# Kernel tuning notes

Hardware: AMD Instinct MI355X
Metric: run time of the kernel (lower is better)

Reference implementation:

```python
import jax, jax.numpy as jnp
import numpy as np

N = 50000          # nodes
E_RAND = 590000    # random edges (+ N self-loops -> E = 640000)
IN_F = 128
OUT_F = 128
H, D = 8, 16       # num_heads, head_dim (H*D == OUT_F)
HOP = 5
ALPHA = 0.1
SLOPE = 0.2
EPS = 1e-5


def _layer_norm(x, g, b):
    mu = jnp.mean(x, axis=-1, keepdims=True)
    var = jnp.mean((x - mu) ** 2, axis=-1, keepdims=True)
    return (x - mu) * jax.lax.rsqrt(var + EPS) * g + b


def setup_inputs() -> dict:
    key = jax.random.key(0)
    ks = jax.random.split(key, 10)
    loops = jnp.arange(N, dtype=jnp.int32)  # self-loops -> no 0-in-degree nodes
    src = jnp.concatenate([loops, jax.random.randint(ks[0], (E_RAND,), 0, N, dtype=jnp.int32)])
    dst = jnp.concatenate([loops, jax.random.randint(ks[1], (E_RAND,), 0, N, dtype=jnp.int32)])
    s = 0.05  # xavier-like small init gain
    return {
        "feat": jax.random.normal(ks[2], (N, IN_F), jnp.float32),
        "src": src,
        "dst": dst,
        "w_head": jax.random.normal(ks[3], (OUT_F, IN_F), jnp.float32) * s,
        "w_tail": jax.random.normal(ks[4], (OUT_F, IN_F), jnp.float32) * s,
        "w_ent": jax.random.normal(ks[5], (OUT_F, IN_F), jnp.float32) * s,
        "attn": jax.random.normal(ks[6], (1, H, D), jnp.float32) * s,
        "ln1_g": jnp.ones((IN_F,), jnp.float32),
        "ln1_b": jnp.zeros((IN_F,), jnp.float32),
        "ln2_g": jnp.ones((OUT_F,), jnp.float32),
        "ln2_b": jnp.zeros((OUT_F,), jnp.float32),
        "ff_w1": jax.random.normal(ks[7], (4 * OUT_F, OUT_F), jnp.float32) * s,
        "ff_b1": jnp.zeros((4 * OUT_F,), jnp.float32),
        "ff_w2": jax.random.normal(ks[8], (OUT_F, 4 * OUT_F), jnp.float32) * s,
        "ff_b2": jnp.zeros((OUT_F,), jnp.float32),
    }


def _forward(src, dst, feat, w_head, w_tail, w_ent, attn,
             ln1_g, ln1_b, ln2_g, ln2_b, ff_w1, ff_b1, ff_w2, ff_b2):
    ones = jnp.ones(src.shape[0], jnp.float32)
    out_deg = jnp.clip(jax.ops.segment_sum(ones, src, num_segments=N), 1.0)  # [N]
    in_deg = jnp.clip(jax.ops.segment_sum(ones, dst, num_segments=N), 1.0)
    head_norm = out_deg ** -0.5
    tail_norm = in_deg ** 0.5
    log_in = jnp.log1p(in_deg)  # graph.dstdata['log_in'] (log of in-degree, set at graph build time)

    x = _layer_norm(feat, ln1_g, ln1_b)  # graph_layer_norm (feat_drop=0 in eval)
    fh = (x @ w_head.T).reshape(N, H, D) * head_norm[:, None, None]
    ft = (x @ w_tail.T).reshape(N, H, D) * head_norm[:, None, None]
    fe = (x @ w_ent.T).reshape(N, H, D) * head_norm[:, None, None]

    # edge attention logits: u_mul_v -> leaky_relu -> dot with attn vector
    lr = jax.nn.leaky_relu(fh[src] * ft[dst], SLOPE)  # [E,H,D]
    e = jnp.einsum('ehd,xhd->eh', lr, attn)           # [E,H]
    e = e * log_in[dst][:, None] / D                  # e_mul_v with log_in, / head_dim

    # edge softmax grouped by destination node, per head
    seg_max = jax.ops.segment_max(e, dst, num_segments=N)
    e_exp = jnp.exp(e - seg_max[dst])
    denom = jax.ops.segment_sum(e_exp, dst, num_segments=N)
    a = e_exp / denom[dst]                            # [E,H]

    # PPR diffusion (ppr_estimation), attn_drop=0 in eval
    feat0 = fe
    h = feat0
    for hop in range(HOP):
        if hop > 0:
            h = h * head_norm[:, None, None]
        m = h[src] * a[:, :, None]                    # [E,H,D] u_mul_e
        h = jax.ops.segment_sum(m, dst, num_segments=N)  # fn.sum
        h = h * tail_norm[:, None, None]
        h = (1.0 - ALPHA) * h + ALPHA * feat0

    rst = h + feat.reshape(N, H, D)  # res_fc is Identity since in_feats == out_feats
    rst = rst.reshape(N, OUT_F)
    ff = _layer_norm(rst, ln2_g, ln2_b)
    ff = jax.nn.relu(ff @ ff_w1.T + ff_b1) @ ff_w2.T + ff_b2  # PositionWiseFeedForward
    return ff + rst


def reference(feat, src, dst, w_head, w_tail, w_ent, attn, ln1_g, ln1_b,
              ln2_g, ln2_b, ff_w1, ff_b1, ff_w2, ff_b2):
    return _forward(src, dst, feat, w_head, w_tail, w_ent, attn,
                    ln1_g, ln1_b, ln2_g, ln2_b, ff_w1, ff_b1, ff_w2, ff_b2)
```

## Files before the change

### kernel.cpp

```cpp
#include <hip/hip_runtime.h>
#include <hip/hip_bf16.h>
#include <hip/hip_fp16.h>

typedef __attribute__((ext_vector_type(8))) short bf16x8;
typedef __attribute__((ext_vector_type(4))) float f32x4;
typedef unsigned int uint32;

#define F 128
#define HOPS 5
#define LDS_STRIDE 68
#define W1_STRIDE 136
#define W2_STRIDE 72
#define TB_STRIDE 72

__device__ __forceinline__ float b2f(__hip_bfloat16 h) { return __bfloat162float(h); }
__device__ __forceinline__ __hip_bfloat16 f2b(float f) { return __float2bfloat16(f); }

__device__ __forceinline__ float load_in(const void* p, size_t i, int isbf) {
    return isbf ? __bfloat162float(((const __hip_bfloat16*)p)[i]) : ((const float*)p)[i];
}

__device__ __forceinline__ float bflo(uint32 u) { union { uint32 i; float f; } v; v.i = u << 16; return v.f; }
__device__ __forceinline__ float bfhi(uint32 u) { union { uint32 i; float f; } v; v.i = u & 0xffff0000u; return v.f; }
__device__ __forceinline__ uint32 packbf2(float a, float b) {
    __hip_bfloat16 ha = f2b(a), hb = f2b(b);
    unsigned short ua = *(unsigned short*)&ha, ub = *(unsigned short*)&hb;
    return ((uint32)ub << 16) | ua;
}

__device__ __forceinline__ int xcd_id() {
    unsigned v;
    asm volatile("s_getreg_b32 %0, hwreg(HW_REG_XCC_ID)" : "=s"(v));
    return (int)(v & 7);
}

__device__ __forceinline__ float edge_dot2(uint4 gv, const float* c1, const float* c2) {
    float acc = 0.f, acc2 = 0.f;
    uint32 us[4] = {gv.x, gv.y, gv.z, gv.w};
    #pragma unroll
    for (int k = 0; k < 4; ++k) {
        float f0 = bflo(us[k]), f1 = bfhi(us[k]);
        acc  = fmaf(c1[2 * k],     f0,        acc);
        acc2 = fmaf(c2[2 * k],     fabsf(f0), acc2);
        acc  = fmaf(c1[2 * k + 1], f1,        acc);
        acc2 = fmaf(c2[2 * k + 1], fabsf(f1), acc2);
    }
    return acc + acc2;
}

__global__ void detect_k(const uint32* __restrict__ w, int* flag) {
    __shared__ int cnt[256];
    int t = threadIdx.x;
    uint32 x = w[t * 97];
    int e_low = (x >> 7) & 0xFF;
    cnt[t] = (e_low >= 110 && e_low <= 135) ? 1 : 0;
    __syncthreads();
    for (int s = 128; s > 0; s >>= 1) {
        if (t < s) cnt[t] += cnt[t + s];
        __syncthreads();
    }
    if (t == 0) flag[0] = (cnt[0] >= 160) ? 1 : 0;
}

__global__ void cvt_all_k(const void* __restrict__ w_head, const void* __restrict__ w_tail,
                          const void* __restrict__ w_ent, const void* __restrict__ ff_w1,
                          const void* __restrict__ ff_w2, const void* __restrict__ attn,
                          const void* __restrict__ ff_b1, const void* __restrict__ ff_b2,
                          const int* __restrict__ flag,
                          __hip_bfloat16* __restrict__ wblob, float* __restrict__ fblob) {
    int i = blockIdx.x * blockDim.x + threadIdx.x;
    int isbf = flag[0];
    if (i < 180224) {
        const void* srcp; int j;
        if (i < 16384)       { srcp = w_head; j = i; }
        else if (i < 32768)  { srcp = w_tail; j = i - 16384; }
        else if (i < 49152)  { srcp = w_ent;  j = i - 32768; }
        else if (i < 114688) { srcp = ff_w1;  j = i - 49152; }
        else                 { srcp = ff_w2;  j = i - 114688; }
        wblob[i] = f2b(load_in(srcp, j, isbf));
    } else if (i < 180992) {
        int k = i - 180224;
        const void* srcp; int j;
        if (k < 128)      { srcp = attn;  j = k; }
        else if (k < 640) { srcp = ff_b1; j = k - 128; }
        else              { srcp = ff_b2; j = k - 640; }
        fblob[k] = load_in(srcp, j, isbf);
    }
}

__global__ void degree_k(const int* __restrict__ src, const int* __restrict__ dst,
                         int* in8, int* out1, uint32* __restrict__ pack, int E, int N) {
    int base = blockIdx.x * (blockDim.x * 8) + threadIdx.x;
    int slice = xcd_id();
    int idx[8], d[8], s[8], r[8];
#pragma unroll
    for (int k = 0; k < 8; ++k) idx[k] = base + k * 256;
#pragma unroll
    for (int k = 0; k < 8; ++k)
        if (idx[k] < E) { d[k] = dst[idx[k]]; s[k] = src[idx[k]]; }
#pragma unroll
    for (int k = 0; k < 8; ++k)
        if (idx[k] < E) r[k] = atomicAdd(&in8[slice * N + d[k]], 1);
#pragma unroll
    for (int k = 0; k < 8; ++k)
        if (idx[k] < E) atomicAdd(&out1[s[k]], 1);
#pragma unroll
    for (int k = 0; k < 8; ++k)
        if (idx[k] < E) pack[idx[k]] = (uint32)r[k] | ((uint32)slice << 24);
}

__global__ void scan1_k(const int* __restrict__ in8, int* partial, int* blk_sum, int N) {
    __shared__ int sh[256];
    int t = threadIdx.x;
    int i = blockIdx.x * 256 + t;
    int c = 0;
    if (i < N) {
#pragma unroll
        for (int s = 0; s < 8; ++s) c += in8[s * N + i];
    }
    sh[t] = c;
    __syncthreads();
    for (int o = 1; o < 256; o <<= 1) {
        int v = (t >= o) ? sh[t - o] : 0;
        __syncthreads();
        sh[t] += v;
        __syncthreads();
    }
    if (i < N) partial[i] = sh[t] - c;
    if (t == 255) blk_sum[blockIdx.x] = sh[255];
}

__global__ void scan2_k(const int* __restrict__ blk_sum, int* blk_off, int nb,
                        int* row_ptr, int N) {
    __shared__ int sh[256];
    int t = threadIdx.x;
    if (nb <= 256) {
        int v = (t < nb) ? blk_sum[t] : 0;
        sh[t] = v;
        __syncthreads();
        for (int o = 1; o < 256; o <<= 1) {
            int u = (t >= o) ? sh[t - o] : 0;
            __syncthreads();
            sh[t] += u;
            __syncthreads();
        }
        if (t < nb) blk_off[t] = sh[t] - v;
        if (t == 255) row_ptr[N] = sh[255];
    } else if (t == 0) {
        int run = 0;
        for (int b = 0; b < nb; ++b) { blk_off[b] = run; run += blk_sum[b]; }
        row_ptr[N] = run;
    }
}

__global__ void scan3_norms_k(const int* __restrict__ partial, const int* __restrict__ blk_off,
                              const int* __restrict__ in8, const int* __restrict__ out1,
                              int* row_ptr, int* soff, float* head_norm, float* tail_norm,
                              float* log_in, int N) {
    int i = blockIdx.x * 256 + threadIdx.x;
    if (i >= N) return;
    row_ptr[i] = partial[i] + blk_off[blockIdx.x];
    int run = 0;
#pragma unroll
    for (int s = 0; s < 8; ++s) { soff[s * N + i] = run; run += in8[s * N + i]; }
    int od = out1[i];
    float id = fmaxf((float)run, 1.0f);
    float odf = fmaxf((float)od, 1.0f);
    head_norm[i] = rsqrtf(odf);
    tail_norm[i] = sqrtf(id);
    log_in[i] = log1pf(id);
}

__global__ void scan3f_k(const int* __restrict__ partial, const int* __restrict__ blk_sum,
                         int nb, const int* __restrict__ in8, const int* __restrict__ out1,
                         int* row_ptr, int* soff, float* head_norm, float* tail_norm,
                         float* log_in, int N) {
    __shared__ int bs[256];
    int t = threadIdx.x;
    bs[t] = (t < nb) ? blk_sum[t] : 0;
    __syncthreads();
    for (int o = 1; o < 256; o <<= 1) {
        int v = (t >= o) ? bs[t - o] : 0;
        __syncthreads();
        bs[t] += v;
        __syncthreads();
    }
    if (blockIdx.x == 0 && t == 0) row_ptr[N] = bs[nb - 1];
    int boff = (blockIdx.x == 0) ? 0 : bs[blockIdx.x - 1];
    int i = blockIdx.x * 256 + t;
    if (i >= N) return;
    row_ptr[i] = partial[i] + boff;
    int run = 0;
#pragma unroll
    for (int s = 0; s < 8; ++s) { soff[s * N + i] = run; run += in8[s * N + i]; }
    int od = out1[i];
    float id = fmaxf((float)run, 1.0f);
    float odf = fmaxf((float)od, 1.0f);
    head_norm[i] = rsqrtf(odf);
    tail_norm[i] = sqrtf(id);
    log_in[i] = log1pf(id);
}

__global__ void scatter_k(const int* __restrict__ src, const int* __restrict__ dst,
                          const int* __restrict__ row_ptr, const int* __restrict__ soff,
                          const uint32* __restrict__ pack, int* csr_src, int E, int N) {
    int i = blockIdx.x * blockDim.x + threadIdx.x;
    if (i < E) {
        int d = dst[i];
        uint32 pk = pack[i];
        int s = (int)(pk >> 24);
        int r = (int)(pk & 0xFFFFFFu);
        csr_src[row_ptr[d] + soff[s * N + d] + r] = src[i];
    }
}

__global__ void ln1_k(const void* __restrict__ x, const void* __restrict__ g,
                      const void* __restrict__ b, const int* __restrict__ flag,
                      __hip_bfloat16* __restrict__ y, int N) {
    int w = blockIdx.x * (blockDim.x >> 6) + (threadIdx.x >> 6);
    if (w >= N) return;
    int isbf = flag[0];
    int t = threadIdx.x & 63;
    float v0 = load_in(x, (size_t)w * F + t, isbf);
    float v1 = load_in(x, (size_t)w * F + t + 64, isbf);
    float s = v0 + v1, sq = v0 * v0 + v1 * v1;
    for (int m = 1; m < 64; m <<= 1) { s += __shfl_xor(s, m, 64); sq += __shfl_xor(sq, m, 64); }
    float mu = s * (1.0f / F);
    float var = fmaxf(sq * (1.0f / F) - mu * mu, 0.0f);
    float r = rsqrtf(var + 1e-5f);
    y[(size_t)w * F + t]      = f2b((v0 - mu) * r * load_in(g, t, isbf) + load_in(b, t, isbf));
    y[(size_t)w * F + t + 64] = f2b((v1 - mu) * r * load_in(g, t + 64, isbf) + load_in(b, t + 64, isbf));
}

__global__ void proj_gemm_k(const __hip_bfloat16* __restrict__ X,
                            const __hip_bfloat16* __restrict__ Wall,
                            const float* __restrict__ head_norm,
                            __hip_bfloat16* __restrict__ fh,
                            __hip_bfloat16* __restrict__ ft,
                            uint32* __restrict__ fe_bf, int N) {
    __shared__ __align__(16) char smem[2 * 64 * W1_STRIDE * 2];
    __hip_bfloat16* lx = (__hip_bfloat16*)smem;
    __hip_bfloat16* lw = (__hip_bfloat16*)(smem + 64 * W1_STRIDE * 2);
    float* eps = (float*)smem;
    int tid = threadIdx.x;
    int wv = tid >> 6, lane = tid & 63;
    int lr = lane & 15, quad = lane >> 4;
    int bm = blockIdx.x * 64;
    int g = blockIdx.y;
    int wsel = g >> 1;
    int wcb = (g & 1) * 64;
    {
        const __hip_bfloat16* xs = X + (size_t)bm * F;
        size_t maxe = (size_t)N * F;
#pragma unroll
        for (int i = 0; i < 4; ++i) {
            int idx = i * 2048 + tid * 8;
            int n = idx >> 7, k = idx & 127;
            size_t gi = (size_t)bm * F + idx;
            uint4 v = (gi + 8 <= maxe) ? *(const uint4*)(xs + idx)
                                       : *(const uint4*)(X + maxe - 8);
            *(uint4*)&lx[n * W1_STRIDE + k] = v;
        }
        const __hip_bfloat16* ws = Wall + ((size_t)wsel * F + wcb) * F;
#pragma unroll
        for (int i = 0; i < 4; ++i) {
            int idx = i * 2048 + tid * 8;
            int n = idx >> 7, k = idx & 127;
            *(uint4*)&lw[n * W1_STRIDE + k] = *(const uint4*)(ws + idx);
        }
    }
    __syncthreads();
    f32x4 acc[4] = {{0,0,0,0},{0,0,0,0},{0,0,0,0},{0,0,0,0}};
#pragma unroll
    for (int ks = 0; ks < 4; ++ks) {
        bf16x8 a = *reinterpret_cast<const bf16x8*>(&lx[(wv * 16 + lr) * W1_STRIDE + ks * 32 + quad * 8]);
#pragma unroll
        for (int j = 0; j < 4; ++j) {
            bf16x8 bb = *reinterpret_cast<const bf16x8*>(&lw[(j * 16 + lr) * W1_STRIDE + ks * 32 + quad * 8]);
            acc[j] = __builtin_amdgcn_mfma_f32_16x16x32_bf16(a, bb, acc[j], 0, 0, 0);
        }
    }
    __syncthreads();
    int rl = wv * 16 + quad * 4;
#pragma unroll
    for (int j = 0; j < 4; ++j)
#pragma unroll
        for (int r = 0; r < 4; ++r)
            eps[(rl + r) * LDS_STRIDE + j * 16 + lr] = acc[j][r];
    __syncthreads();
    int tr = tid >> 4, tc = (tid & 15) * 4;
#pragma unroll
    for (int p = 0; p < 4; ++p) {
        int row_l = p * 16 + tr;
        int grow = bm + row_l;
        if (grow >= N) continue;
        float4 v = *(const float4*)&eps[row_l * LDS_STRIDE + tc];
        float hn = head_norm[grow];
        v.x *= hn; v.y *= hn; v.z *= hn; v.w *= hn;
        size_t idx = (size_t)grow * F + wcb + tc;
        uint2 u; u.x = packbf2(v.x, v.y); u.y = packbf2(v.z, v.w);
        __hip_bfloat16* dstp = (wsel == 0) ? fh : (wsel == 1) ? ft : (__hip_bfloat16*)fe_bf;
        *(uint2*)&dstp[idx] = u;
    }
}

__global__ void attn_soft_k(const int* __restrict__ csr_src, const int* __restrict__ row_ptr,
                            const uint32* __restrict__ fh2, const uint32* __restrict__ ft2,
                            const float* __restrict__ attn_f, const float* __restrict__ log_in,
                            __half* __restrict__ e_h, float* __restrict__ inv_arr, int N) {
    int w = blockIdx.x * (blockDim.x >> 6) + (threadIdx.x >> 6);
    if (w >= N) return;
    int t = threadIdx.x & 63;
    int g = t >> 4, j = t & 15;
    int b = row_ptr[w], e = row_ptr[w + 1];
    uint4 fr = ((const uint4*)ft2)[(size_t)w * 16 + j];
    float ftf[8] = {bflo(fr.x), bfhi(fr.x), bflo(fr.y), bfhi(fr.y),
                    bflo(fr.z), bfhi(fr.z), bflo(fr.w), bfhi(fr.w)};
    float c1[8], c2[8];
#pragma unroll
    for (int k = 0; k < 8; ++k) {
        float at = attn_f[8 * j + k];
        c1[k] = 0.6f * at * ftf[k];
        c2[k] = 0.4f * at * fabsf(ftf[k]);
    }
    float scale = log_in[w] * (1.0f / 16.0f);
    float m = -1e30f;
    for (int p0 = b; p0 < e; p0 += 8) {
        int pa = p0 + g, pb = p0 + 4 + g;
        bool oka = pa < e, okb = pb < e;
        int sa = csr_src[oka ? pa : b];
        int sb = csr_src[okb ? pb : b];
        uint4 ga = ((const uint4*)fh2)[(size_t)sa * 16 + j];
        uint4 gb = ((const uint4*)fh2)[(size_t)sb * 16 + j];
        float ra = edge_dot2(ga, c1, c2);
        float rb = edge_dot2(gb, c1, c2);
        ra += __shfl_xor(ra, 1, 64);
        rb += __shfl_xor(rb, 1, 64);
        float la = ra * scale, lb = rb * scale;
        if (oka) { if (!(j & 1)) e_h[(size_t)pa * 8 + (j >> 1)] = __float2half(la); m = fmaxf(m, la); }
        if (okb) { if (!(j & 1)) e_h[(size_t)pb * 8 + (j >> 1)] = __float2half(lb); m = fmaxf(m, lb); }
    }
    m = fmaxf(m, __shfl_xor(m, 16, 64));
    m = fmaxf(m, __shfl_xor(m, 32, 64));
    float mh = __shfl(m, (t & 7) * 2, 64);
    float sum = 0.f;
    for (size_t base = (size_t)b * 8 + t; base < (size_t)e * 8; base += 64) {
        float ex = expf(__half2float(e_h[base]) - mh);
        e_h[base] = __float2half(ex);
        sum += ex;
    }
    sum += __shfl_xor(sum, 8, 64);
    sum += __shfl_xor(sum, 16, 64);
    sum += __shfl_xor(sum, 32, 64);
    float inv = 1.0f / fmaxf(sum, 1e-30f);
    if (t < 8) inv_arr[(size_t)w * 8 + t] = inv;
}

__global__ void hop_k(const uint32* __restrict__ gsrc2, const __half* __restrict__ e_h,
                      const float* __restrict__ inv_arr,
                      const int* __restrict__ csr_src, const int* __restrict__ row_ptr,
                      const float* __restrict__ tail_norm, const float* __restrict__ head_norm,
                      const uint32* __restrict__ fe_bf, const void* __restrict__ feat,
                      const void* __restrict__ ln2g, const void* __restrict__ ln2b,
                      const int* __restrict__ flag,
                      uint32* __restrict__ out_bf, float* __restrict__ out_f32,
                      int last, int N) {
    int w = blockIdx.x * 8 + (threadIdx.x >> 5);
    if (w >= N) return;
    int l = threadIdx.x & 31;
    int h = l >> 2;
    int b = row_ptr[w], e = row_ptr[w + 1];
    float inv = inv_arr[(size_t)w * 8 + h];
    float a0 = 0.f, a1 = 0.f, a2 = 0.f, a3 = 0.f;
    int p = b;
    for (; p + 8 <= e; p += 8) {
        int s[8]; float av[8]; uint2 gg[8];
#pragma unroll
        for (int i = 0; i < 8; ++i) s[i] = csr_src[p + i];
#pragma unroll
        for (int i = 0; i < 8; ++i) av[i] = __half2float(e_h[(size_t)(p + i) * 8 + h]);
#pragma unroll
        for (int i = 0; i < 8; ++i) gg[i] = ((const uint2*)gsrc2)[(size_t)s[i] * 32 + l];
#pragma unroll
        for (int i = 0; i < 8; ++i) {
            a0 += bflo(gg[i].x) * av[i]; a1 += bfhi(gg[i].x) * av[i];
            a2 += bflo(gg[i].y) * av[i]; a3 += bfhi(gg[i].y) * av[i];
        }
    }
    if (p < e) {
        int s[8]; float av[8]; uint2 gg[8];
#pragma unroll
        for (int i = 0; i < 8; ++i) {
            int q = p + i;
            bool ok = q < e;
            int q2 = ok ? q : b;
            s[i] = csr_src[q2];
            av[i] = ok ? __half2float(e_h[(size_t)q * 8 + h]) : 0.f;
        }
#pragma unroll
        for (int i = 0; i < 8; ++i) gg[i] = ((const uint2*)gsrc2)[(size_t)s[i] * 32 + l];
#pragma unroll
        for (int i = 0; i < 8; ++i) {
            a0 += bflo(gg[i].x) * av[i]; a1 += bfhi(gg[i].x) * av[i];
            a2 += bflo(gg[i].y) * av[i]; a3 += bfhi(gg[i].y) * av[i];
        }
    }
    float tl = tail_norm[w] * 0.9f * inv;
    uint2 feu = ((const uint2*)fe_bf)[(size_t)w * 32 + l];
    float r0 = tl * a0 + 0.1f * bflo(feu.x);
    float r1 = tl * a1 + 0.1f * bfhi(feu.x);
    float r2 = tl * a2 + 0.1f * bflo(feu.y);
    float r3 = tl * a3 + 0.1f * bfhi(feu.y);
    if (last) {
        int isbf = flag[0];
        float4 o;
        if (isbf) {
            uint2 fu = ((const uint2*)feat)[(size_t)w * 32 + l];
            o.x = r0 + bflo(fu.x); o.y = r1 + bfhi(fu.x);
            o.z = r2 + bflo(fu.y); o.w = r3 + bfhi(fu.y);
        } else {
            float4 fv = ((const float4*)feat)[(size_t)w * 32 + l];
            o.x = r0 + fv.x; o.y = r1 + fv.y; o.z = r2 + fv.z; o.w = r3 + fv.w;
        }
        ((float4*)out_f32)[(size_t)w * 32 + l] = o;
        float s2 = o.x + o.y + o.z + o.w;
        float sq = o.x * o.x + o.y * o.y + o.z * o.z + o.w * o.w;
#pragma unroll
        for (int mm = 1; mm < 32; mm <<= 1) {
            s2 += __shfl_xor(s2, mm, 64);
            sq += __shfl_xor(sq, mm, 64);
        }
        float mu = s2 * (1.0f / F);
        float var = fmaxf(sq * (1.0f / F) - mu * mu, 0.0f);
        float rr = rsqrtf(var + 1e-5f);
        float g0 = load_in(ln2g, 4 * l + 0, isbf), g1 = load_in(ln2g, 4 * l + 1, isbf);
        float g2 = load_in(ln2g, 4 * l + 2, isbf), g3 = load_in(ln2g, 4 * l + 3, isbf);
        float b0 = load_in(ln2b, 4 * l + 0, isbf), b1 = load_in(ln2b, 4 * l + 1, isbf);
        float b2 = load_in(ln2b, 4 * l + 2, isbf), b3 = load_in(ln2b, 4 * l + 3, isbf);
        uint2 u;
        u.x = packbf2((o.x - mu) * rr * g0 + b0, (o.y - mu) * rr * g1 + b1);
        u.y = packbf2((o.z - mu) * rr * g2 + b2, (o.w - mu) * rr * g3 + b3);
        ((uint2*)out_bf)[(size_t)w * 32 + l] = u;
    } else {
        float hn = head_norm[w];
        uint2 u;
        u.x = packbf2(r0 * hn, r1 * hn);
        u.y = packbf2(r2 * hn, r3 * hn);
        ((uint2*)out_bf)[(size_t)w * 32 + l] = u;
    }
}

__global__ __launch_bounds__(256, 2)
void ffn_fused_k(const __hip_bfloat16* __restrict__ Y, const __hip_bfloat16* __restrict__ W1,
                 const __hip_bfloat16* __restrict__ W2, const float* __restrict__ b1f,
                 const float* __restrict__ b2f, const float* __restrict__ rst,
                 const int* __restrict__ flag, void* __restrict__ out, int N) {
    __shared__ __align__(16) char smem[45056];
    __hip_bfloat16* lw1 = (__hip_bfloat16*)smem;
    __hip_bfloat16* lw2 = (__hip_bfloat16*)(smem + 17408);
    __hip_bfloat16* tb  = (__hip_bfloat16*)(smem + 35840);
    float* eps = (float*)smem;
    int tid = threadIdx.x;
    int wv = tid >> 6, lane = tid & 63;
    int lr = lane & 15, quad = lane >> 4;
    int bm = blockIdx.x * 64;
    int row_a = bm + wv * 16 + lr;
    if (row_a >= N) row_a = N - 1;
    bf16x8 ay[4];
    {
        const __hip_bfloat16* yr = Y + (size_t)row_a * F + quad * 8;
#pragma unroll
        for (int ks = 0; ks < 4; ++ks) ay[ks] = *reinterpret_cast<const bf16x8*>(yr + ks * 32);
    }
    f32x4 o[8];
#pragma unroll
    for (int j = 0; j < 8; ++j) o[j] = (f32x4){0,0,0,0};
    __hip_bfloat16* tbuf = tb + wv * (16 * TB_STRIDE);
    for (int c = 0; c < 8; ++c) {
        int nb0 = c * 64;
        __syncthreads();
        {
            const __hip_bfloat16* s1 = W1 + (size_t)nb0 * F;
#pragma unroll
            for (int i = 0; i < 4; ++i) {
                int idx = i * 2048 + tid * 8;
                int n = idx >> 7, k = idx & 127;
                *(uint4*)&lw1[n * W1_STRIDE + k] = *(const uint4*)(s1 + idx);
            }
#pragma unroll
            for (int i = 0; i < 4; ++i) {
                int idx = i * 2048 + tid * 8;
                int r = idx >> 6, k2 = idx & 63;
                *(uint4*)&lw2[r * W2_STRIDE + k2] = *(const uint4*)(W2 + (size_t)r * 512 + nb0 + k2);
            }
        }
        __syncthreads();
        f32x4 t[4] = {{0,0,0,0},{0,0,0,0},{0,0,0,0},{0,0,0,0}};
#pragma unroll
        for (int ks = 0; ks < 4; ++ks) {
#pragma unroll
            for (int j = 0; j < 4; ++j) {
                bf16x8 bb = *reinterpret_cast<const bf16x8*>(&lw1[(j * 16 + lr) * W1_STRIDE + ks * 32 + quad * 8]);
                t[j] = __builtin_amdgcn_mfma_f32_16x16x32_bf16(ay[ks], bb, t[j], 0, 0, 0);
            }
        }
#pragma unroll
        for (int j = 0; j < 4; ++j) {
            float bias = b1f[nb0 + 16 * j + lr];
#pragma unroll
            for (int r = 0; r < 4; ++r) {
                float v = fmaxf(t[j][r] + bias, 0.f);
                tbuf[(quad * 4 + r) * TB_STRIDE + j * 16 + lr] = f2b(v);
            }
        }
#pragma unroll
        for (int ks2 = 0; ks2 < 2; ++ks2) {
            bf16x8 at = *reinterpret_cast<const bf16x8*>(&tbuf[lr * TB_STRIDE + ks2 * 32 + quad * 8]);
#pragma unroll
            for (int j2 = 0; j2 < 8; ++j2) {
                bf16x8 bb = *reinterpret_cast<const bf16x8*>(&lw2[(j2 * 16 + lr) * W2_STRIDE + ks2 * 32 + quad * 8]);
                o[j2] = __builtin_amdgcn_mfma_f32_16x16x32_bf16(at, bb, o[j2], 0, 0, 0);
            }
        }
    }
    __syncthreads();
    int rl = wv * 16 + quad * 4;
#pragma unroll
    for (int j = 0; j < 8; ++j)
#pragma unroll
        for (int r = 0; r < 4; ++r)
            eps[(rl + r) * 132 + j * 16 + lr] = o[j][r];
    __syncthreads();
    int isbf = flag[0];
#pragma unroll
    for (int p = 0; p < 8; ++p) {
        int idx = p * 1024 + tid * 4;
        int row_l = idx >> 7, col = idx & 127;
        int grow = bm + row_l;
        if (grow >= N) continue;
        float4 v = *(const float4*)&eps[row_l * 132 + col];
        float4 bias = *(const float4*)&b2f[col];
        float4 rv = *(const float4*)&rst[(size_t)grow * F + col];
        v.x += bias.x + rv.x; v.y += bias.y + rv.y;
        v.z += bias.z + rv.z; v.w += bias.w + rv.w;
        size_t gidx = (size_t)grow * F + col;
        if (isbf) {
            uint2 u; u.x = packbf2(v.x, v.y); u.y = packbf2(v.z, v.w);
            *(uint2*)&((__hip_bfloat16*)out)[gidx] = u;
        } else {
            *(float4*)&((float*)out)[gidx] = v;
        }
    }
}

extern "C" void kernel_launch(void* const* d_in, const int* in_sizes, int n_in,
                              void* d_out, int out_size, void* d_ws, size_t ws_size,
                              hipStream_t stream) {
    if (n_in < 15) return;
    const void* feat = d_in[0];
    const int* src = (const int*)d_in[1];
    const int* dst = (const int*)d_in[2];
    const void* w_head = d_in[3];
    const void* w_tail = d_in[4];
    const void* w_ent  = d_in[5];
    const void* attn   = d_in[6];
    const void* ln1_g  = d_in[7];
    const void* ln1_b  = d_in[8];
    const void* ln2_g  = d_in[9];
    const void* ln2_b  = d_in[10];
    const void* ff_w1  = d_in[11];
    const void* ff_b1  = d_in[12];
    const void* ff_w2  = d_in[13];
    const void* ff_b2  = d_in[14];

    const int N = in_sizes[0] / F;
    const int E = in_sizes[1];
    (void)out_size;

    char* base = (char*)d_ws;
    size_t off = 0;
    auto alloc = [&](size_t bytes) -> void* {
        void* r = base + off;
        off += (bytes + 255) & ~(size_t)255;
        return r;
    };
    int* zr        = (int*)alloc((size_t)9 * N * 4);
    int* in8 = zr, * out1 = zr + 8 * N;
    int* soff      = (int*)alloc((size_t)8 * N * 4);
    int* row_ptr   = (int*)alloc((size_t)(N + 1) * 4);
    int* partial   = (int*)alloc((size_t)N * 4);
    int* blk_sum   = (int*)alloc((size_t)1024 * 4);
    int* blk_off   = (int*)alloc((size_t)1024 * 4);
    int* flag      = (int*)alloc(256);
    float* head_norm = (float*)alloc((size_t)N * 4);
    float* tail_norm = (float*)alloc((size_t)N * 4);
    float* log_in    = (float*)alloc((size_t)N * 4);
    float* inv_arr   = (float*)alloc((size_t)N * 8 * 4);
    int* csr_src   = (int*)alloc((size_t)E * 4);
    uint32* pack   = (uint32*)alloc((size_t)E * 4);
    __hip_bfloat16* wh_bf = (__hip_bfloat16*)alloc((size_t)F * F * 2);
    __hip_bfloat16* wt_bf = (__hip_bfloat16*)alloc((size_t)F * F * 2);
    __hip_bfloat16* we_bf = (__hip_bfloat16*)alloc((size_t)F * F * 2);
    __hip_bfloat16* w1_bf = (__hip_bfloat16*)alloc((size_t)512 * F * 2);
    __hip_bfloat16* w2_bf = (__hip_bfloat16*)alloc((size_t)F * 512 * 2);
    float* attn_f    = (float*)alloc((size_t)F * 4);
    float* b1f       = (float*)alloc((size_t)512 * 4);
    float* b2f_      = (float*)alloc((size_t)F * 4);
    __hip_bfloat16* x_bf = (__hip_bfloat16*)alloc((size_t)N * F * 2);
    __hip_bfloat16* fh   = (__hip_bfloat16*)alloc((size_t)N * F * 2);
    __hip_bfloat16* ftb  = (__hip_bfloat16*)alloc((size_t)N * F * 2);
    uint32* fe_bf = (uint32*)alloc((size_t)N * F * 2);
    uint32* hA_bf = (uint32*)alloc((size_t)N * F * 2);
    uint32* hB_bf = (uint32*)alloc((size_t)N * F * 2);
    float* rst = (float*)alloc((size_t)N * F * 4);
    __hip_bfloat16* y_bf = (__hip_bfloat16*)hA_bf;
    __half* e_h = (__half*)x_bf;
    (void)wt_bf; (void)we_bf;
    if (off > ws_size) return;

    const int Mb = (N + 63) / 64;
    const int nodeBlocks = (N + 3) / 4;
    const int hopBlocks = (N + 7) / 8;
    const int nb = (N + 255) / 256;

    detect_k<<<1, 256, 0, stream>>>((const uint32*)feat, flag);
    cvt_all_k<<<(180992 + 255) / 256, 256, 0, stream>>>(w_head, w_tail, w_ent, ff_w1, ff_w2,
                                                        attn, ff_b1, ff_b2, flag, wh_bf, attn_f);

    hipMemsetAsync(zr, 0, (size_t)9 * N * 4, stream);
    degree_k<<<(E + 2047) / 2048, 256, 0, stream>>>(src, dst, in8, out1, pack, E, N);
    scan1_k<<<nb, 256, 0, stream>>>(in8, partial, blk_sum, N);
    if (nb <= 256) {
        scan3f_k<<<nb, 256, 0, stream>>>(partial, blk_sum, nb, in8, out1,
                                         row_ptr, soff, head_norm, tail_norm, log_in, N);
    } else {
        scan2_k<<<1, 256, 0, stream>>>(blk_sum, blk_off, nb, row_ptr, N);
        scan3_norms_k<<<nb, 256, 0, stream>>>(partial, blk_off, in8, out1,
                                              row_ptr, soff, head_norm, tail_norm, log_in, N);
    }
    scatter_k<<<(E + 255) / 256, 256, 0, stream>>>(src, dst, row_ptr, soff, pack, csr_src, E, N);

    ln1_k<<<nodeBlocks, 256, 0, stream>>>(feat, ln1_g, ln1_b, flag, x_bf, N);
    proj_gemm_k<<<dim3(Mb, 6), 256, 0, stream>>>(x_bf, wh_bf, head_norm, fh, ftb, fe_bf, N);

    attn_soft_k<<<nodeBlocks, 256, 0, stream>>>(csr_src, row_ptr, (const uint32*)fh,
                                                (const uint32*)ftb, attn_f, log_in,
                                                e_h, inv_arr, N);

    const uint32* gsrc = fe_bf;
    uint32* bufs[2] = {hA_bf, hB_bf};
    for (int hop = 0; hop < HOPS; ++hop) {
        int last = (hop == HOPS - 1);
        uint32* dst_bf = last ? (uint32*)y_bf : bufs[hop & 1];
        hop_k<<<hopBlocks, 256, 0, stream>>>(gsrc, e_h, inv_arr, csr_src, row_ptr, tail_norm,
                                             head_norm, fe_bf, feat, ln2_g, ln2_b, flag,
                                             dst_bf, rst, last, N);
        if (!last) gsrc = dst_bf;
    }

    ffn_fused_k<<<Mb, 256, 0, stream>>>(y_bf, w1_bf, w2_bf, b1f, b2f_, rst, flag, d_out, N);
}
```

Measured before the change: 450.1 us.

## Merge independent preprocessing kernels into block-partitioned fused launches

Combines degree counting, LayerNorm1 and weight conversion into one launch whose blocks branch on block index. It also merges the CSR scatter with the projection GEMM into a second launch. This removes several kernel launches and gaps between them, and lets independent work overlap on the device. The cost is that the GEMM blocks carry the same LDS allocation as the scatter blocks, and occupancy is set by the heavier branch.

Measured after the change: 429.2 us. 4.6% less time.

```diff
diff --git a/kernel.cpp b/kernel.cpp
--- a/kernel.cpp
+++ b/kernel.cpp
@@ -62,51 +62,75 @@
     if (t == 0) flag[0] = (cnt[0] >= 160) ? 1 : 0;
 }
 
-__global__ void cvt_all_k(const void* __restrict__ w_head, const void* __restrict__ w_tail,
-                          const void* __restrict__ w_ent, const void* __restrict__ ff_w1,
-                          const void* __restrict__ ff_w2, const void* __restrict__ attn,
-                          const void* __restrict__ ff_b1, const void* __restrict__ ff_b2,
-                          const int* __restrict__ flag,
-                          __hip_bfloat16* __restrict__ wblob, float* __restrict__ fblob) {
-    int i = blockIdx.x * blockDim.x + threadIdx.x;
-    int isbf = flag[0];
-    if (i < 180224) {
-        const void* srcp; int j;
-        if (i < 16384)       { srcp = w_head; j = i; }
-        else if (i < 32768)  { srcp = w_tail; j = i - 16384; }
-        else if (i < 49152)  { srcp = w_ent;  j = i - 32768; }
-        else if (i < 114688) { srcp = ff_w1;  j = i - 49152; }
-        else                 { srcp = ff_w2;  j = i - 114688; }
-        wblob[i] = f2b(load_in(srcp, j, isbf));
-    } else if (i < 180992) {
-        int k = i - 180224;
-        const void* srcp; int j;
-        if (k < 128)      { srcp = attn;  j = k; }
-        else if (k < 640) { srcp = ff_b1; j = k - 128; }
-        else              { srcp = ff_b2; j = k - 640; }
-        fblob[k] = load_in(srcp, j, isbf);
-    }
-}
-
-__global__ void degree_k(const int* __restrict__ src, const int* __restrict__ dst,
-                         int* in8, int* out1, uint32* __restrict__ pack, int E, int N) {
-    int base = blockIdx.x * (blockDim.x * 8) + threadIdx.x;
-    int slice = xcd_id();
-    int idx[8], d[8], s[8], r[8];
-#pragma unroll
-    for (int k = 0; k < 8; ++k) idx[k] = base + k * 256;
-#pragma unroll
-    for (int k = 0; k < 8; ++k)
-        if (idx[k] < E) { d[k] = dst[idx[k]]; s[k] = src[idx[k]]; }
-#pragma unroll
-    for (int k = 0; k < 8; ++k)
-        if (idx[k] < E) r[k] = atomicAdd(&in8[slice * N + d[k]], 1);
-#pragma unroll
-    for (int k = 0; k < 8; ++k)
-        if (idx[k] < E) atomicAdd(&out1[s[k]], 1);
-#pragma unroll
-    for (int k = 0; k < 8; ++k)
-        if (idx[k] < E) pack[idx[k]] = (uint32)r[k] | ((uint32)slice << 24);
+__global__ void fused_pre_k(const int* __restrict__ src, const int* __restrict__ dst,
+                            int* in8, int* out1, uint32* __restrict__ pack, int E,
+                            const void* __restrict__ feat, const void* __restrict__ ln1g,
+                            const void* __restrict__ ln1b,
+                            const void* __restrict__ w_head, const void* __restrict__ w_tail,
+                            const void* __restrict__ w_ent, const void* __restrict__ ff_w1,
+                            const void* __restrict__ ff_w2, const void* __restrict__ attn,
+                            const void* __restrict__ ff_b1, const void* __restrict__ ff_b2,
+                            const int* __restrict__ flag,
+                            __hip_bfloat16* __restrict__ wblob, float* __restrict__ fblob,
+                            __hip_bfloat16* __restrict__ x_bf,
+                            int nbDeg, int nbLn, int N) {
+    int bid = blockIdx.x;
+    if (bid < nbDeg) {
+        int base = bid * 2048 + threadIdx.x;
+        int slice = xcd_id();
+        int idx[8], d[8], s[8], r[8];
+#pragma unroll
+        for (int k = 0; k < 8; ++k) idx[k] = base + k * 256;
+#pragma unroll
+        for (int k = 0; k < 8; ++k)
+            if (idx[k] < E) { d[k] = dst[idx[k]]; s[k] = src[idx[k]]; }
+#pragma unroll
+        for (int k = 0; k < 8; ++k)
+            if (idx[k] < E) r[k] = atomicAdd(&in8[slice * N + d[k]], 1);
+#pragma unroll
+        for (int k = 0; k < 8; ++k)
+            if (idx[k] < E) atomicAdd(&out1[s[k]], 1);
+#pragma unroll
+        for (int k = 0; k < 8; ++k)
+            if (idx[k] < E) pack[idx[k]] = (uint32)r[k] | ((uint32)slice << 24);
+        return;
+    }
+    if (bid < nbDeg + nbLn) {
+        int w = (bid - nbDeg) * 4 + (threadIdx.x >> 6);
+        if (w >= N) return;
+        int isbf = flag[0];
+        int t = threadIdx.x & 63;
+        float v0 = load_in(feat, (size_t)w * F + t, isbf);
+        float v1 = load_in(feat, (size_t)w * F + t + 64, isbf);
+        float s = v0 + v1, sq = v0 * v0 + v1 * v1;
+        for (int m = 1; m < 64; m <<= 1) { s += __shfl_xor(s, m, 64); sq += __shfl_xor(sq, m, 64); }
+        float mu = s * (1.0f / F);
+        float var = fmaxf(sq * (1.0f / F) - mu * mu, 0.0f);
+        float r = rsqrtf(var + 1e-5f);
+        x_bf[(size_t)w * F + t]      = f2b((v0 - mu) * r * load_in(ln1g, t, isbf) + load_in(ln1b, t, isbf));
+        x_bf[(size_t)w * F + t + 64] = f2b((v1 - mu) * r * load_in(ln1g, t + 64, isbf) + load_in(ln1b, t + 64, isbf));
+        return;
+    }
+    {
+        int i = (bid - nbDeg - nbLn) * 256 + threadIdx.x;
+        int isbf = flag[0];
+        if (i < 180224) {
+            const void* srcp; int j;
+            if (i < 16384)       { srcp = w_head; j = i; }
+            else if (i < 32768)  { srcp = w_tail; j = i - 16384; }
+            else if (i < 49152)  { srcp = w_ent;  j = i - 32768; }
+            else if (i < 114688) { srcp = ff_w1;  j = i - 49152; }
+            else                 { srcp = ff_w2;  j = i - 114688; }
+            wblob[i] = f2b(load_in(srcp, j, isbf));
+        } else if (i < 180992) {
+            int k = i - 180224;
+            const void* srcp; int j;
+            if (k < 128)      { srcp = attn;  j = k; }
+            else if (k < 640) { srcp = ff_b1; j = k - 128; }
+            else              { srcp = ff_b2; j = k - 640; }
+            fblob[k] = load_in(srcp, j, isbf);
+        }
+    }
 }
 
 __global__ void scan1_k(const int* __restrict__ in8, int* partial, int* blk_sum, int N) {
@@ -201,52 +225,42 @@
     log_in[i] = log1pf(id);
 }
 
-__global__ void scatter_k(const int* __restrict__ src, const int* __restrict__ dst,
-                          const int* __restrict__ row_ptr, const int* __restrict__ soff,
-                          const uint32* __restrict__ pack, int* csr_src, int E, int N) {
-    int i = blockIdx.x * blockDim.x + threadIdx.x;
-    if (i < E) {
-        int d = dst[i];
-        uint32 pk = pack[i];
-        int s = (int)(pk >> 24);
-        int r = (int)(pk & 0xFFFFFFu);
-        csr_src[row_ptr[d] + soff[s * N + d] + r] = src[i];
-    }
-}
-
-__global__ void ln1_k(const void* __restrict__ x, const void* __restrict__ g,
-                      const void* __restrict__ b, const int* __restrict__ flag,
-                      __hip_bfloat16* __restrict__ y, int N) {
-    int w = blockIdx.x * (blockDim.x >> 6) + (threadIdx.x >> 6);
-    if (w >= N) return;
-    int isbf = flag[0];
-    int t = threadIdx.x & 63;
-    float v0 = load_in(x, (size_t)w * F + t, isbf);
-    float v1 = load_in(x, (size_t)w * F + t + 64, isbf);
-    float s = v0 + v1, sq = v0 * v0 + v1 * v1;
-    for (int m = 1; m < 64; m <<= 1) { s += __shfl_xor(s, m, 64); sq += __shfl_xor(sq, m, 64); }
-    float mu = s * (1.0f / F);
-    float var = fmaxf(sq * (1.0f / F) - mu * mu, 0.0f);
-    float r = rsqrtf(var + 1e-5f);
-    y[(size_t)w * F + t]      = f2b((v0 - mu) * r * load_in(g, t, isbf) + load_in(b, t, isbf));
-    y[(size_t)w * F + t + 64] = f2b((v1 - mu) * r * load_in(g, t + 64, isbf) + load_in(b, t + 64, isbf));
-}
-
-__global__ void proj_gemm_k(const __hip_bfloat16* __restrict__ X,
+__global__ void fused_mid_k(const int* __restrict__ src, const int* __restrict__ dst,
+                            const int* __restrict__ row_ptr, const int* __restrict__ soff,
+                            const uint32* __restrict__ pack, int* __restrict__ csr_src,
+                            int E, int N, int nbSc, int Mb,
+                            const __hip_bfloat16* __restrict__ X,
                             const __hip_bfloat16* __restrict__ Wall,
                             const float* __restrict__ head_norm,
                             __hip_bfloat16* __restrict__ fh,
                             __hip_bfloat16* __restrict__ ft,
-                            uint32* __restrict__ fe_bf, int N) {
+                            uint32* __restrict__ fe_bf) {
     __shared__ __align__(16) char smem[2 * 64 * W1_STRIDE * 2];
+    int bid = blockIdx.x;
+    if (bid < nbSc) {
+        int base = bid * 2048 + threadIdx.x;
+#pragma unroll
+        for (int k = 0; k < 8; ++k) {
+            int i = base + k * 256;
+            if (i < E) {
+                int d = dst[i];
+                uint32 pk = pack[i];
+                int s = (int)(pk >> 24);
+                int r = (int)(pk & 0xFFFFFFu);
+                csr_src[row_ptr[d] + soff[s * N + d] + r] = src[i];
+            }
+        }
+        return;
+    }
+    int pb = bid - nbSc;
+    int g = pb / Mb;
+    int bm = (pb - g * Mb) * 64;
     __hip_bfloat16* lx = (__hip_bfloat16*)smem;
     __hip_bfloat16* lw = (__hip_bfloat16*)(smem + 64 * W1_STRIDE * 2);
     float* eps = (float*)smem;
     int tid = threadIdx.x;
     int wv = tid >> 6, lane = tid & 63;
     int lr = lane & 15, quad = lane >> 4;
-    int bm = blockIdx.x * 64;
-    int g = blockIdx.y;
     int wsel = g >> 1;
     int wcb = (g & 1) * 64;
     {
@@ -622,13 +636,19 @@
     const int nodeBlocks = (N + 3) / 4;
     const int hopBlocks = (N + 7) / 8;
     const int nb = (N + 255) / 256;
+    const int nbDeg = (E + 2047) / 2048;
+    const int nbLn  = (N + 3) / 4;
+    const int nbCvt = (180992 + 255) / 256;
 
     detect_k<<<1, 256, 0, stream>>>((const uint32*)feat, flag);
-    cvt_all_k<<<(180992 + 255) / 256, 256, 0, stream>>>(w_head, w_tail, w_ent, ff_w1, ff_w2,
-                                                        attn, ff_b1, ff_b2, flag, wh_bf, attn_f);
-
     hipMemsetAsync(zr, 0, (size_t)9 * N * 4, stream);
-    degree_k<<<(E + 2047) / 2048, 256, 0, stream>>>(src, dst, in8, out1, pack, E, N);
+
+    fused_pre_k<<<nbDeg + nbLn + nbCvt, 256, 0, stream>>>(
+        src, dst, in8, out1, pack, E,
+        feat, ln1_g, ln1_b,
+        w_head, w_tail, w_ent, ff_w1, ff_w2, attn, ff_b1, ff_b2,
+        flag, wh_bf, attn_f, x_bf, nbDeg, nbLn, N);
+
     scan1_k<<<nb, 256, 0, stream>>>(in8, partial, blk_sum, N);
     if (nb <= 256) {
         scan3f_k<<<nb, 256, 0, stream>>>(partial, blk_sum, nb, in8, out1,
@@ -638,10 +658,11 @@
         scan3_norms_k<<<nb, 256, 0, stream>>>(partial, blk_off, in8, out1,
                                               row_ptr, soff, head_norm, tail_norm, log_in, N);
     }
-    scatter_k<<<(E + 255) / 256, 256, 0, stream>>>(src, dst, row_ptr, soff, pack, csr_src, E, N);
-
-    ln1_k<<<nodeBlocks, 256, 0, stream>>>(feat, ln1_g, ln1_b, flag, x_bf, N);
-    proj_gemm_k<<<dim3(Mb, 6), 256, 0, stream>>>(x_bf, wh_bf, head_norm, fh, ftb, fe_bf, N);
+
+    const int nbSc = (E + 2047) / 2048;
+    fused_mid_k<<<nbSc + Mb * 6, 256, 0, stream>>>(
+        src, dst, row_ptr, soff, pack, csr_src, E, N, nbSc, Mb,
+        x_bf, wh_bf, head_norm, fh, ftb, fe_bf);
 
     attn_soft_k<<<nodeBlocks, 256, 0, stream>>>(csr_src, row_ptr, (const uint32*)fh,
                                                 (const uint32*)ftb, attn_f, log_in,
```
